# Performance work log

Measured on AMD Instinct MI355X. Metric: run time of the kernel, lower is better.

## Reference

```python
import jax, jax.numpy as jnp
import numpy as np

B, K, H, E = 16384, 5, 512, 512


def setup_inputs() -> dict:
    key = jax.random.key(0)
    ks = jax.random.split(key, 6)
    return {
        "query": jax.random.normal(ks[0], (B, H), dtype=jnp.float32),
        "topics": jax.random.normal(ks[1], (B, K, E), dtype=jnp.float32),
        "coverage_vector": jax.random.uniform(ks[2], (B, K), dtype=jnp.float32),
        "Ua": jax.random.normal(ks[3], (H, E), dtype=jnp.float32) * (1.0 / np.sqrt(E)),
        "Wa": jax.random.normal(ks[4], (H, H), dtype=jnp.float32) * (1.0 / np.sqrt(H)),
        "va_w": jax.random.normal(ks[5], (1, H), dtype=jnp.float32) * (1.0 / np.sqrt(H)),
        "va_b": jnp.zeros((1,), dtype=jnp.float32),
    }


def reference(query, topics, coverage_vector, Ua, Wa, va_w, va_b):
    # proj_key for all topics at once: [B, K, H]
    proj_keys = jnp.einsum("bke,he->bkh", topics, Ua)
    # Faithful to original: query is re-projected by Wa each loop iteration,
    # so step i uses Wa^(i+1) @ query.
    q = query
    scores = []
    for i in range(topics.shape[1]):  # K is small & fixed (topics)
        q = q @ Wa.T  # [B, H]
        s = jnp.tanh(q + proj_keys[:, i, :]) @ va_w.T + va_b  # [B, 1]
        scores.append(s[:, 0] * coverage_vector[:, i])  # [B]
    scores = jnp.stack(scores, axis=1)  # [B, K]
    alphas = jax.nn.softmax(scores, axis=1)  # [B, K]
    mt = jnp.einsum("bk,bke->be", alphas, topics)  # [B, E]
    return (mt, alphas)
```

## Files before the change

kernel.cpp:

```cpp
#include <hip/hip_runtime.h>
#include <hip/hip_bf16.h>
#include <stdint.h>

#define B_SZ 16384
#define K_SZ 5
#define H_SZ 512
#define E_SZ 512

typedef _Float16 f16;
typedef _Float16 f16x8 __attribute__((ext_vector_type(8)));
typedef float    f32x4 __attribute__((ext_vector_type(4)));

__device__ __forceinline__ void gload_lds16(const void* g, void* l) {
  __builtin_amdgcn_global_load_lds(
      (const __attribute__((address_space(1))) unsigned int*)g,
      (__attribute__((address_space(3))) unsigned int*)l, 16, 0, 0);
}

__device__ __forceinline__ float fast_tanh(float x) {
  float e = __expf(-2.f * fabsf(x));
  float r = (1.f - e) / (1.f + e);
  return copysignf(r, x);
}

__global__ __launch_bounds__(256)
void prep_all(const float* __restrict__ Wa, const float* __restrict__ Ua,
              const float* __restrict__ query, f16* __restrict__ Wbig0,
              f16* __restrict__ Ua_h, f16* __restrict__ WaT,
              f16* __restrict__ q0h, unsigned* __restrict__ bar) {
  const int t = threadIdx.x;
  const int bb = blockIdx.x;
  if (bb == 0 && t == 0) *bar = 0u;
  if (bb < 128) {
    size_t o = ((size_t)bb * 256 + t) * 8;
    float4 a = *(const float4*)(Wa + o);
    float4 b = *(const float4*)(Wa + o + 4);
    union { f16 h[8]; uint4 u; } u;
    u.h[0] = (f16)a.x; u.h[1] = (f16)a.y; u.h[2] = (f16)a.z; u.h[3] = (f16)a.w;
    u.h[4] = (f16)b.x; u.h[5] = (f16)b.y; u.h[6] = (f16)b.z; u.h[7] = (f16)b.w;
    *(uint4*)(Wbig0 + o) = u.u;
  } else if (bb < 256) {
    size_t o = ((size_t)(bb - 128) * 256 + t) * 8;
    float4 a = *(const float4*)(Ua + o);
    float4 b = *(const float4*)(Ua + o + 4);
    union { f16 h[8]; uint4 u; } u;
    u.h[0] = (f16)a.x; u.h[1] = (f16)a.y; u.h[2] = (f16)a.z; u.h[3] = (f16)a.w;
    u.h[4] = (f16)b.x; u.h[5] = (f16)b.y; u.h[6] = (f16)b.z; u.h[7] = (f16)b.w;
    *(uint4*)(Ua_h + o) = u.u;
  } else if (bb < 512) {
    __shared__ float tile[32][33];
    int blk = bb - 256;
    int bx = blk & 15, by = blk >> 4;
    int tx = t & 31, ty = t >> 5;
    #pragma unroll
    for (int i = 0; i < 32; i += 8)
      tile[ty + i][tx] = Wa[(size_t)(by * 32 + ty + i) * 512 + bx * 32 + tx];
    __syncthreads();
    #pragma unroll
    for (int i = 0; i < 32; i += 8)
      WaT[(size_t)(bx * 32 + ty + i) * 512 + by * 32 + tx] =
          (f16)tile[tx][ty + i];
  } else {
    size_t o = ((size_t)(bb - 512) * 256 + t) * 8;
    float4 a = *(const float4*)(query + o);
    float4 b = *(const float4*)(query + o + 4);
    union { f16 h[8]; uint4 u; } u;
    u.h[0] = (f16)a.x; u.h[1] = (f16)a.y; u.h[2] = (f16)a.z; u.h[3] = (f16)a.w;
    u.h[4] = (f16)b.x; u.h[5] = (f16)b.y; u.h[6] = (f16)b.z; u.h[7] = (f16)b.w;
    *(uint4*)(q0h + o) = u.u;
  }
}

__device__ __forceinline__ void gbar(unsigned* cnt, unsigned target) {
  __syncthreads();
  if (threadIdx.x == 0) {
    __threadfence();
    __hip_atomic_fetch_add(cnt, 1u, __ATOMIC_ACQ_REL, __HIP_MEMORY_SCOPE_AGENT);
    while (__hip_atomic_load(cnt, __ATOMIC_ACQUIRE,
                             __HIP_MEMORY_SCOPE_AGENT) < target)
      __builtin_amdgcn_s_sleep(2);
    __threadfence();
  }
  __syncthreads();
}

__global__ __launch_bounds__(256)
void power_chain(const f16* __restrict__ WaT, f16* __restrict__ Wbig,
                 unsigned* __restrict__ bar) {
  __shared__ f16 As[128 * 32];
  __shared__ f16 Bs[128 * 32];
  const int t = threadIdx.x, l = t & 63, wid = t >> 6;
  const int wm = wid >> 1, wn = wid & 1;
  const int mt = blockIdx.x >> 2, nt = blockIdx.x & 3;
  const int m0 = mt * 128, n0 = nt * 128;
  const int lrow = l & 15, lk = (l >> 4) * 8;

  for (int j = 1; j < K_SZ; ++j) {
    const f16* A = Wbig + (size_t)(j - 1) * (512 * 512);
    f16* Y = Wbig + (size_t)j * (512 * 512);
    f32x4 acc[4][4] = {};
    for (int k0 = 0; k0 < 512; k0 += 32) {
      #pragma unroll
      for (int p = 0; p < 2; ++p) {
        int c = p * 256 + t, row = c >> 2, seg = c & 3;
        gload_lds16(WaT + (size_t)(n0 + row) * 512 + k0 + seg * 8,
                    (char*)Bs + c * 16);
        gload_lds16(A + (size_t)(m0 + row) * 512 + k0 + seg * 8,
                    (char*)As + c * 16);
      }
      __syncthreads();
      f16x8 af[4], bf[4];
      #pragma unroll
      for (int mi = 0; mi < 4; ++mi)
        af[mi] = *(const f16x8*)(As + (wm * 64 + mi * 16 + lrow) * 32 + lk);
      #pragma unroll
      for (int ni = 0; ni < 4; ++ni)
        bf[ni] = *(const f16x8*)(Bs + (wn * 64 + ni * 16 + lrow) * 32 + lk);
      #pragma unroll
      for (int mi = 0; mi < 4; ++mi)
        #pragma unroll
        for (int ni = 0; ni < 4; ++ni)
          acc[mi][ni] = __builtin_amdgcn_mfma_f32_16x16x32_f16(
              af[mi], bf[ni], acc[mi][ni], 0, 0, 0);
      __syncthreads();
    }
    #pragma unroll
    for (int mi = 0; mi < 4; ++mi)
      #pragma unroll
      for (int j2 = 0; j2 < 4; ++j2) {
        size_t row = m0 + wm * 64 + mi * 16 + ((l >> 4) << 2) + j2;
        #pragma unroll
        for (int ni = 0; ni < 4; ++ni)
          Y[row * 512 + n0 + wn * 64 + ni * 16 + lrow] = (f16)acc[mi][ni][j2];
      }
    if (j < K_SZ - 1) gbar(bar, 16u * (unsigned)j);
  }
}

__global__ __launch_bounds__(256)
void fused_score_gemm(const float* __restrict__ topics,
                      const f16* __restrict__ q0h,
                      const f16* __restrict__ Ua_h,
                      const f16* __restrict__ Wbig,
                      const float* __restrict__ va_w,
                      float* __restrict__ partials) {
  __shared__ f16 As[2][128 * 32];
  __shared__ f16 Bs[2][128 * 32];
  const int t = threadIdx.x;
  const int l = t & 63, wid = t >> 6;
  const int wm = wid >> 1, wn = wid & 1;
  int bid = blockIdx.x;
  const int nwg = gridDim.x;
  bid = (bid & 7) * (nwg >> 3) + (bid >> 3);
  const int kq = bid >> 9;
  const int rem = bid & 511;
  const int mt = rem >> 2, nt = rem & 3;
  const size_t m0 = (size_t)mt * 128;
  const int n0 = nt * 128;
  const int lrow = l & 15;
  const int lk = (l >> 4) * 8;
  const f16* Pk = Wbig + (size_t)kq * (512 * 512);

  const float* tA = topics + ((m0 + (t >> 3)) * K_SZ + kq) * (size_t)E_SZ +
                    (t & 7) * 4;
  const int ldsA1 = (t >> 3) * 64 + (t & 7) * 8;
  const f16* tB1 = Ua_h + (size_t)(n0 + (t >> 2)) * 512 + (t & 3) * 8;
  const f16* tB2 = Pk + (size_t)(n0 + (t >> 2)) * 512 + (t & 3) * 8;
  const f16* tA2 = q0h + (m0 + (t >> 2)) * (size_t)H_SZ + (t & 3) * 8;

  float4 areg[4];
  f32x4 acc[4][4] = {};

  auto stage1 = [&](int k0, int buf) {
    #pragma unroll
    for (int p = 0; p < 2; ++p)
      gload_lds16(tB1 + (size_t)p * 64 * 512 + k0,
                  (char*)Bs[buf] + (p * 256 + t) * 16);
    #pragma unroll
    for (int p = 0; p < 4; ++p)
      areg[p] = *(const float4*)(tA + (size_t)p * 32 * K_SZ * E_SZ + k0);
  };
  auto write1 = [&](int buf) {
    #pragma unroll
    for (int p = 0; p < 4; ++p) {
      union { f16 h[4]; uint2 u; } cv;
      cv.h[0] = (f16)areg[p].x; cv.h[1] = (f16)areg[p].y;
      cv.h[2] = (f16)areg[p].z; cv.h[3] = (f16)areg[p].w;
      *(uint2*)((char*)As[buf] + p * 2048 + ldsA1) = cv.u;
    }
  };
  auto stage2 = [&](int k0, int buf) {
    #pragma unroll
    for (int p = 0; p < 2; ++p) {
      gload_lds16(tB2 + (size_t)p * 64 * 512 + k0,
                  (char*)Bs[buf] + (p * 256 + t) * 16);
      gload_lds16(tA2 + (size_t)p * 64 * H_SZ + k0,
                  (char*)As[buf] + (p * 256 + t) * 16);
    }
  };
  auto compute = [&](int buf) {
    f16x8 af[4], bf[4];
    #pragma unroll
    for (int mi = 0; mi < 4; ++mi)
      af[mi] = *(const f16x8*)(As[buf] + (wm * 64 + mi * 16 + lrow) * 32 + lk);
    #pragma unroll
    for (int ni = 0; ni < 4; ++ni)
      bf[ni] = *(const f16x8*)(Bs[buf] + (wn * 64 + ni * 16 + lrow) * 32 + lk);
    #pragma unroll
    for (int mi = 0; mi < 4; ++mi)
      #pragma unroll
      for (int ni = 0; ni < 4; ++ni)
        acc[mi][ni] = __builtin_amdgcn_mfma_f32_16x16x32_f16(
            af[mi], bf[ni], acc[mi][ni], 0, 0, 0);
  };

  stage1(0, 0);
  write1(0);
  __syncthreads();

  #pragma unroll 2
  for (int i = 0; i < 16; ++i) {
    const int cur = i & 1;
    if (i < 15) stage1((i + 1) * 32, cur ^ 1);
    else        stage2(0, cur ^ 1);
    compute(cur);
    if (i < 15) write1(cur ^ 1);
    __syncthreads();
  }
  #pragma unroll 2
  for (int i = 0; i < 16; ++i) {
    const int cur = i & 1;
    if (i < 15) stage2((i + 1) * 32, cur ^ 1);
    compute(cur);
    __syncthreads();
  }

  const int colbase = n0 + wn * 64 + lrow;
  float va4[4];
  #pragma unroll
  for (int ni = 0; ni < 4; ++ni) va4[ni] = va_w[colbase + ni * 16];

  #pragma unroll
  for (int mi = 0; mi < 4; ++mi) {
    #pragma unroll
    for (int j = 0; j < 4; ++j) {
      float s = 0.f;
      #pragma unroll
      for (int ni = 0; ni < 4; ++ni)
        s += va4[ni] * fast_tanh(acc[mi][ni][j]);
      #pragma unroll
      for (int m = 1; m < 16; m <<= 1) s += __shfl_xor(s, m);
      if (lrow == 0) {
        int row = (int)m0 + wm * 64 + mi * 16 + ((l >> 4) << 2) + j;
        partials[(size_t)(nt * 2 + wn) * (K_SZ * B_SZ) + kq * B_SZ + row] = s;
      }
    }
  }
}

__global__ __launch_bounds__(256)
void finalize2(const float* __restrict__ partials,
               const float* __restrict__ topics, const float* __restrict__ cov,
               const float* __restrict__ va_b, float* __restrict__ out) {
  const int wid = threadIdx.x >> 6, l = threadIdx.x & 63;
  const size_t b = (size_t)blockIdx.x * 4 + wid;
  const float vb = va_b[0];

  float s[K_SZ];
  #pragma unroll
  for (int k = 0; k < K_SZ; ++k) {
    float raw = 0.f;
    #pragma unroll
    for (int sl = 0; sl < 8; ++sl)
      raw += partials[(size_t)sl * (K_SZ * B_SZ) + k * B_SZ + b];
    s[k] = (raw + vb) * cov[b * K_SZ + k];
  }

  float m = s[0];
  #pragma unroll
  for (int k = 1; k < K_SZ; ++k) m = fmaxf(m, s[k]);
  float a[K_SZ], d = 0.f;
  #pragma unroll
  for (int k = 0; k < K_SZ; ++k) { a[k] = __expf(s[k] - m); d += a[k]; }
  float inv = 1.f / d;
  #pragma unroll
  for (int k = 0; k < K_SZ; ++k) a[k] *= inv;

  float acc0[4] = {}, acc1[4] = {};
  #pragma unroll
  for (int k = 0; k < K_SZ; ++k) {
    const float* tp = topics + (b * K_SZ + k) * E_SZ + l * 8;
    float4 t0 = *(const float4*)tp;
    float4 t1 = *(const float4*)(tp + 4);
    acc0[0] += a[k] * t0.x; acc0[1] += a[k] * t0.y;
    acc0[2] += a[k] * t0.z; acc0[3] += a[k] * t0.w;
    acc1[0] += a[k] * t1.x; acc1[1] += a[k] * t1.y;
    acc1[2] += a[k] * t1.z; acc1[3] += a[k] * t1.w;
  }
  float* mo = out + b * E_SZ + l * 8;
  *(float4*)mo       = make_float4(acc0[0], acc0[1], acc0[2], acc0[3]);
  *(float4*)(mo + 4) = make_float4(acc1[0], acc1[1], acc1[2], acc1[3]);
  if (l < K_SZ) {
    float av = (l == 0) ? a[0] : (l == 1) ? a[1] : (l == 2) ? a[2]
               : (l == 3) ? a[3] : a[4];
    out[(size_t)B_SZ * E_SZ + b * K_SZ + l] = av;
  }
}

extern "C" void kernel_launch(void* const* d_in, const int* in_sizes, int n_in,
                              void* d_out, int out_size, void* d_ws, size_t ws_size,
                              hipStream_t stream) {
  const float* query  = (const float*)d_in[0];
  const float* topics = (const float*)d_in[1];
  const float* cov    = (const float*)d_in[2];
  const float* Ua     = (const float*)d_in[3];
  const float* Wa     = (const float*)d_in[4];
  const float* va_w   = (const float*)d_in[5];
  const float* va_b   = (const float*)d_in[6];
  float* out = (float*)d_out;

  char* ws = (char*)d_ws;
  size_t off = 0;
  auto alloc = [&](size_t bytes) -> char* {
    char* p = ws + off;
    off += (bytes + 255) & ~(size_t)255;
    return p;
  };
  f16* q0h   = (f16*)alloc((size_t)B_SZ * H_SZ * 2);
  f16* Ua_h  = (f16*)alloc((size_t)H_SZ * E_SZ * 2);
  f16* WaT   = (f16*)alloc((size_t)H_SZ * H_SZ * 2);
  f16* Wbig  = (f16*)alloc((size_t)K_SZ * H_SZ * H_SZ * 2);
  float* partials = (float*)alloc((size_t)8 * K_SZ * B_SZ * 4);
  unsigned* bar   = (unsigned*)alloc(256);

  prep_all<<<4608, 256, 0, stream>>>(Wa, Ua, query, Wbig, Ua_h, WaT, q0h, bar);
  power_chain<<<16, 256, 0, stream>>>(WaT, Wbig, bar);
  fused_score_gemm<<<K_SZ * (B_SZ / 128) * (H_SZ / 128), 256, 0, stream>>>(
      topics, q0h, Ua_h, Wbig, va_w, partials);
  finalize2<<<B_SZ / 4, 256, 0, stream>>>(partials, topics, cov, va_b, out);
}
```

Baseline: 481.0 us.

## Split-K Wa power chain across 256 blocks and pre-convert topics to fp16

The serial 16-block power chain that computed Wa^2..Wa^5 is replaced by a 256-block split-K scheme with fp32 partial buffers, reductions and global barriers. It also uses repeated squaring (Wa^2 transposed, then Wa^3 and Wa^4, then Wa^5), which cuts the chain to three dependent GEMM levels. Topics are converted to fp16 once in the prep kernel, so the score GEMM can use direct global-to-LDS loads and finalize reads half the bytes. The score GEMM loses its double buffering in exchange, and the extra fp16 topics pass adds traffic. Rounding topics to fp16 also lowers the precision of the mt output.

```diff
diff --git a/kernel.cpp b/kernel.cpp
--- a/kernel.cpp
+++ b/kernel.cpp
@@ -6,6 +6,7 @@
 #define K_SZ 5
 #define H_SZ 512
 #define E_SZ 512
+#define MSZ (512 * 512)
 
 typedef _Float16 f16;
 typedef _Float16 f16x8 __attribute__((ext_vector_type(8)));
@@ -23,30 +24,30 @@
   return copysignf(r, x);
 }
 
+__device__ __forceinline__ void cvt8(const float* src, f16* dst) {
+  float4 a = *(const float4*)src;
+  float4 b = *(const float4*)(src + 4);
+  union { f16 h[8]; uint4 u; } u;
+  u.h[0] = (f16)a.x; u.h[1] = (f16)a.y; u.h[2] = (f16)a.z; u.h[3] = (f16)a.w;
+  u.h[4] = (f16)b.x; u.h[5] = (f16)b.y; u.h[6] = (f16)b.z; u.h[7] = (f16)b.w;
+  *(uint4*)dst = u.u;
+}
+
 __global__ __launch_bounds__(256)
 void prep_all(const float* __restrict__ Wa, const float* __restrict__ Ua,
-              const float* __restrict__ query, f16* __restrict__ Wbig0,
-              f16* __restrict__ Ua_h, f16* __restrict__ WaT,
-              f16* __restrict__ q0h, unsigned* __restrict__ bar) {
+              const float* __restrict__ query, const float* __restrict__ topics,
+              f16* __restrict__ Wbig0, f16* __restrict__ Ua_h,
+              f16* __restrict__ WaT, f16* __restrict__ q0h,
+              f16* __restrict__ topics_h, unsigned* __restrict__ bar) {
   const int t = threadIdx.x;
   const int bb = blockIdx.x;
   if (bb == 0 && t == 0) *bar = 0u;
   if (bb < 128) {
     size_t o = ((size_t)bb * 256 + t) * 8;
-    float4 a = *(const float4*)(Wa + o);
-    float4 b = *(const float4*)(Wa + o + 4);
-    union { f16 h[8]; uint4 u; } u;
-    u.h[0] = (f16)a.x; u.h[1] = (f16)a.y; u.h[2] = (f16)a.z; u.h[3] = (f16)a.w;
-    u.h[4] = (f16)b.x; u.h[5] = (f16)b.y; u.h[6] = (f16)b.z; u.h[7] = (f16)b.w;
-    *(uint4*)(Wbig0 + o) = u.u;
+    cvt8(Wa + o, Wbig0 + o);
   } else if (bb < 256) {
     size_t o = ((size_t)(bb - 128) * 256 + t) * 8;
-    float4 a = *(const float4*)(Ua + o);
-    float4 b = *(const float4*)(Ua + o + 4);
-    union { f16 h[8]; uint4 u; } u;
-    u.h[0] = (f16)a.x; u.h[1] = (f16)a.y; u.h[2] = (f16)a.z; u.h[3] = (f16)a.w;
-    u.h[4] = (f16)b.x; u.h[5] = (f16)b.y; u.h[6] = (f16)b.z; u.h[7] = (f16)b.w;
-    *(uint4*)(Ua_h + o) = u.u;
+    cvt8(Ua + o, Ua_h + o);
   } else if (bb < 512) {
     __shared__ float tile[32][33];
     int blk = bb - 256;
@@ -60,14 +61,12 @@
     for (int i = 0; i < 32; i += 8)
       WaT[(size_t)(bx * 32 + ty + i) * 512 + by * 32 + tx] =
           (f16)tile[tx][ty + i];
+  } else if (bb < 4608) {
+    size_t o = ((size_t)(bb - 512) * 256 + t) * 8;
+    cvt8(query + o, q0h + o);
   } else {
-    size_t o = ((size_t)(bb - 512) * 256 + t) * 8;
-    float4 a = *(const float4*)(query + o);
-    float4 b = *(const float4*)(query + o + 4);
-    union { f16 h[8]; uint4 u; } u;
-    u.h[0] = (f16)a.x; u.h[1] = (f16)a.y; u.h[2] = (f16)a.z; u.h[3] = (f16)a.w;
-    u.h[4] = (f16)b.x; u.h[5] = (f16)b.y; u.h[6] = (f16)b.z; u.h[7] = (f16)b.w;
-    *(uint4*)(q0h + o) = u.u;
+    size_t o = ((size_t)(bb - 4608) * 256 + t) * 8;
+    cvt8(topics + o, topics_h + o);
   }
 }
 
@@ -85,25 +84,28 @@
 }
 
 __global__ __launch_bounds__(256)
-void power_chain(const f16* __restrict__ WaT, f16* __restrict__ Wbig,
+void power_split(f16* __restrict__ Wbig, const f16* __restrict__ WaT,
+                 f16* __restrict__ W2T, float* __restrict__ part,
                  unsigned* __restrict__ bar) {
   __shared__ f16 As[128 * 32];
   __shared__ f16 Bs[128 * 32];
   const int t = threadIdx.x, l = t & 63, wid = t >> 6;
   const int wm = wid >> 1, wn = wid & 1;
-  const int mt = blockIdx.x >> 2, nt = blockIdx.x & 3;
-  const int m0 = mt * 128, n0 = nt * 128;
   const int lrow = l & 15, lk = (l >> 4) * 8;
-
-  for (int j = 1; j < K_SZ; ++j) {
-    const f16* A = Wbig + (size_t)(j - 1) * (512 * 512);
-    f16* Y = Wbig + (size_t)j * (512 * 512);
+  const int bid = blockIdx.x;
+  float* p0 = part;
+  float* p1 = part + (size_t)8 * MSZ;
+
+  auto spk = [&](const f16* A, const f16* W, float* P, int blk) {
+    const int tile = blk >> 3, ks = blk & 7;
+    const int m0 = (tile >> 2) * 128, n0 = (tile & 3) * 128;
     f32x4 acc[4][4] = {};
-    for (int k0 = 0; k0 < 512; k0 += 32) {
+    for (int ki = 0; ki < 2; ++ki) {
+      const int k0 = ks * 64 + ki * 32;
       #pragma unroll
       for (int p = 0; p < 2; ++p) {
         int c = p * 256 + t, row = c >> 2, seg = c & 3;
-        gload_lds16(WaT + (size_t)(n0 + row) * 512 + k0 + seg * 8,
+        gload_lds16(W + (size_t)(n0 + row) * 512 + k0 + seg * 8,
                     (char*)Bs + c * 16);
         gload_lds16(A + (size_t)(m0 + row) * 512 + k0 + seg * 8,
                     (char*)As + c * 16);
@@ -124,28 +126,68 @@
               af[mi], bf[ni], acc[mi][ni], 0, 0, 0);
       __syncthreads();
     }
+    float* Ps = P + (size_t)ks * MSZ;
     #pragma unroll
     for (int mi = 0; mi < 4; ++mi)
       #pragma unroll
-      for (int j2 = 0; j2 < 4; ++j2) {
-        size_t row = m0 + wm * 64 + mi * 16 + ((l >> 4) << 2) + j2;
+      for (int j = 0; j < 4; ++j) {
+        int row = m0 + wm * 64 + mi * 16 + ((l >> 4) << 2) + j;
         #pragma unroll
         for (int ni = 0; ni < 4; ++ni)
-          Y[row * 512 + n0 + wn * 64 + ni * 16 + lrow] = (f16)acc[mi][ni][j2];
+          Ps[(size_t)row * 512 + n0 + wn * 64 + ni * 16 + lrow] =
+              acc[mi][ni][j];
       }
-    if (j < K_SZ - 1) gbar(bar, 16u * (unsigned)j);
-  }
+  };
+  auto reduceg = [&](const float* P, f16* D, int blk) {
+    const int base = (blk * 256 + t) * 8;
+    float s[8] = {};
+    #pragma unroll
+    for (int sl = 0; sl < 8; ++sl) {
+      const float* q = P + (size_t)sl * MSZ + base;
+      float4 a = *(const float4*)q;
+      float4 b = *(const float4*)(q + 4);
+      s[0] += a.x; s[1] += a.y; s[2] += a.z; s[3] += a.w;
+      s[4] += b.x; s[5] += b.y; s[6] += b.z; s[7] += b.w;
+    }
+    union { f16 h[8]; uint4 u; } cv;
+    #pragma unroll
+    for (int j = 0; j < 8; ++j) cv.h[j] = (f16)s[j];
+    *(uint4*)(D + base) = cv.u;
+  };
+
+  f16* Wa1 = Wbig;
+  f16* Wa2 = Wbig + MSZ;
+  f16* Wa3 = Wbig + 2 * (size_t)MSZ;
+  f16* Wa4 = Wbig + 3 * (size_t)MSZ;
+  f16* Wa5 = Wbig + 4 * (size_t)MSZ;
+  unsigned tg = 0;
+
+  if (bid < 128) spk(Wa1, WaT, p0, bid);
+  else           spk(WaT, Wa1, p1, bid - 128);
+  gbar(bar, tg += 256);
+  if (bid < 128) reduceg(p0, Wa2, bid);
+  else           reduceg(p1, W2T, bid - 128);
+  gbar(bar, tg += 256);
+  if (bid < 128) spk(Wa2, WaT, p0, bid);
+  else           spk(Wa2, W2T, p1, bid - 128);
+  gbar(bar, tg += 256);
+  if (bid < 128) reduceg(p0, Wa3, bid);
+  else           reduceg(p1, Wa4, bid - 128);
+  gbar(bar, tg += 256);
+  if (bid < 128) spk(Wa4, WaT, p0, bid);
+  gbar(bar, tg += 256);
+  if (bid < 128) reduceg(p0, Wa5, bid);
 }
 
 __global__ __launch_bounds__(256)
-void fused_score_gemm(const float* __restrict__ topics,
+void fused_score_gemm(const f16* __restrict__ topics_h,
                       const f16* __restrict__ q0h,
                       const f16* __restrict__ Ua_h,
                       const f16* __restrict__ Wbig,
                       const float* __restrict__ va_w,
                       float* __restrict__ partials) {
-  __shared__ f16 As[2][128 * 32];
-  __shared__ f16 Bs[2][128 * 32];
+  __shared__ f16 As[128 * 32];
+  __shared__ f16 Bs[128 * 32];
   const int t = threadIdx.x;
   const int l = t & 63, wid = t >> 6;
   const int wm = wid >> 1, wn = wid & 1;
@@ -159,53 +201,24 @@
   const int n0 = nt * 128;
   const int lrow = l & 15;
   const int lk = (l >> 4) * 8;
-  const f16* Pk = Wbig + (size_t)kq * (512 * 512);
-
-  const float* tA = topics + ((m0 + (t >> 3)) * K_SZ + kq) * (size_t)E_SZ +
-                    (t & 7) * 4;
-  const int ldsA1 = (t >> 3) * 64 + (t & 7) * 8;
-  const f16* tB1 = Ua_h + (size_t)(n0 + (t >> 2)) * 512 + (t & 3) * 8;
-  const f16* tB2 = Pk + (size_t)(n0 + (t >> 2)) * 512 + (t & 3) * 8;
-  const f16* tA2 = q0h + (m0 + (t >> 2)) * (size_t)H_SZ + (t & 3) * 8;
-
-  float4 areg[4];
+  const f16* Pk = Wbig + (size_t)kq * MSZ;
+
+  const int srow = t >> 2, sseg = (t & 3) * 8;
+  const f16* tA1 = topics_h + ((m0 + srow) * K_SZ + kq) * (size_t)E_SZ + sseg;
+  const f16* tB1 = Ua_h + (size_t)(n0 + srow) * 512 + sseg;
+  const f16* tA2 = q0h + (m0 + srow) * (size_t)H_SZ + sseg;
+  const f16* tB2 = Pk + (size_t)(n0 + srow) * 512 + sseg;
+
   f32x4 acc[4][4] = {};
 
-  auto stage1 = [&](int k0, int buf) {
-    #pragma unroll
-    for (int p = 0; p < 2; ++p)
-      gload_lds16(tB1 + (size_t)p * 64 * 512 + k0,
-                  (char*)Bs[buf] + (p * 256 + t) * 16);
-    #pragma unroll
-    for (int p = 0; p < 4; ++p)
-      areg[p] = *(const float4*)(tA + (size_t)p * 32 * K_SZ * E_SZ + k0);
-  };
-  auto write1 = [&](int buf) {
-    #pragma unroll
-    for (int p = 0; p < 4; ++p) {
-      union { f16 h[4]; uint2 u; } cv;
-      cv.h[0] = (f16)areg[p].x; cv.h[1] = (f16)areg[p].y;
-      cv.h[2] = (f16)areg[p].z; cv.h[3] = (f16)areg[p].w;
-      *(uint2*)((char*)As[buf] + p * 2048 + ldsA1) = cv.u;
-    }
-  };
-  auto stage2 = [&](int k0, int buf) {
-    #pragma unroll
-    for (int p = 0; p < 2; ++p) {
-      gload_lds16(tB2 + (size_t)p * 64 * 512 + k0,
-                  (char*)Bs[buf] + (p * 256 + t) * 16);
-      gload_lds16(tA2 + (size_t)p * 64 * H_SZ + k0,
-                  (char*)As[buf] + (p * 256 + t) * 16);
-    }
-  };
-  auto compute = [&](int buf) {
+  auto compute = [&]() {
     f16x8 af[4], bf[4];
     #pragma unroll
     for (int mi = 0; mi < 4; ++mi)
-      af[mi] = *(const f16x8*)(As[buf] + (wm * 64 + mi * 16 + lrow) * 32 + lk);
+      af[mi] = *(const f16x8*)(As + (wm * 64 + mi * 16 + lrow) * 32 + lk);
     #pragma unroll
     for (int ni = 0; ni < 4; ++ni)
-      bf[ni] = *(const f16x8*)(Bs[buf] + (wn * 64 + ni * 16 + lrow) * 32 + lk);
+      bf[ni] = *(const f16x8*)(Bs + (wn * 64 + ni * 16 + lrow) * 32 + lk);
     #pragma unroll
     for (int mi = 0; mi < 4; ++mi)
       #pragma unroll
@@ -214,24 +227,28 @@
             af[mi], bf[ni], acc[mi][ni], 0, 0, 0);
   };
 
-  stage1(0, 0);
-  write1(0);
-  __syncthreads();
-
-  #pragma unroll 2
-  for (int i = 0; i < 16; ++i) {
-    const int cur = i & 1;
-    if (i < 15) stage1((i + 1) * 32, cur ^ 1);
-    else        stage2(0, cur ^ 1);
-    compute(cur);
-    if (i < 15) write1(cur ^ 1);
-    __syncthreads();
-  }
-  #pragma unroll 2
-  for (int i = 0; i < 16; ++i) {
-    const int cur = i & 1;
-    if (i < 15) stage2((i + 1) * 32, cur ^ 1);
-    compute(cur);
+  for (int k0 = 0; k0 < 512; k0 += 32) {
+    #pragma unroll
+    for (int p = 0; p < 2; ++p) {
+      gload_lds16(tB1 + (size_t)p * 64 * 512 + k0,
+                  (char*)Bs + (p * 256 + t) * 16);
+      gload_lds16(tA1 + (size_t)p * 64 * (K_SZ * E_SZ) + k0,
+                  (char*)As + (p * 256 + t) * 16);
+    }
+    __syncthreads();
+    compute();
+    __syncthreads();
+  }
+  for (int k0 = 0; k0 < 512; k0 += 32) {
+    #pragma unroll
+    for (int p = 0; p < 2; ++p) {
+      gload_lds16(tB2 + (size_t)p * 64 * 512 + k0,
+                  (char*)Bs + (p * 256 + t) * 16);
+      gload_lds16(tA2 + (size_t)p * 64 * H_SZ + k0,
+                  (char*)As + (p * 256 + t) * 16);
+    }
+    __syncthreads();
+    compute();
     __syncthreads();
   }
 
@@ -260,7 +277,7 @@
 
 __global__ __launch_bounds__(256)
 void finalize2(const float* __restrict__ partials,
-               const float* __restrict__ topics, const float* __restrict__ cov,
+               const f16* __restrict__ topics_h, const float* __restrict__ cov,
                const float* __restrict__ va_b, float* __restrict__ out) {
   const int wid = threadIdx.x >> 6, l = threadIdx.x & 63;
   const size_t b = (size_t)blockIdx.x * 4 + wid;
@@ -286,20 +303,16 @@
   #pragma unroll
   for (int k = 0; k < K_SZ; ++k) a[k] *= inv;
 
-  float acc0[4] = {}, acc1[4] = {};
+  float accv[8] = {};
   #pragma unroll
   for (int k = 0; k < K_SZ; ++k) {
-    const float* tp = topics + (b * K_SZ + k) * E_SZ + l * 8;
-    float4 t0 = *(const float4*)tp;
-    float4 t1 = *(const float4*)(tp + 4);
-    acc0[0] += a[k] * t0.x; acc0[1] += a[k] * t0.y;
-    acc0[2] += a[k] * t0.z; acc0[3] += a[k] * t0.w;
-    acc1[0] += a[k] * t1.x; acc1[1] += a[k] * t1.y;
-    acc1[2] += a[k] * t1.z; acc1[3] += a[k] * t1.w;
+    f16x8 tv = *(const f16x8*)(topics_h + (b * K_SZ + k) * E_SZ + l * 8);
+    #pragma unroll
+    for (int j = 0; j < 8; ++j) accv[j] += a[k] * (float)tv[j];
   }
   float* mo = out + b * E_SZ + l * 8;
-  *(float4*)mo       = make_float4(acc0[0], acc0[1], acc0[2], acc0[3]);
-  *(float4*)(mo + 4) = make_float4(acc1[0], acc1[1], acc1[2], acc1[3]);
+  *(float4*)mo       = make_float4(accv[0], accv[1], accv[2], accv[3]);
+  *(float4*)(mo + 4) = make_float4(accv[4], accv[5], accv[6], accv[7]);
   if (l < K_SZ) {
     float av = (l == 0) ? a[0] : (l == 1) ? a[1] : (l == 2) ? a[2]
                : (l == 3) ? a[3] : a[4];
@@ -326,16 +339,20 @@
     off += (bytes + 255) & ~(size_t)255;
     return p;
   };
-  f16* q0h   = (f16*)alloc((size_t)B_SZ * H_SZ * 2);
-  f16* Ua_h  = (f16*)alloc((size_t)H_SZ * E_SZ * 2);
-  f16* WaT   = (f16*)alloc((size_t)H_SZ * H_SZ * 2);
-  f16* Wbig  = (f16*)alloc((size_t)K_SZ * H_SZ * H_SZ * 2);
+  f16* topics_h = (f16*)alloc((size_t)B_SZ * K_SZ * E_SZ * 2);
+  f16* q0h      = (f16*)alloc((size_t)B_SZ * H_SZ * 2);
+  f16* Ua_h     = (f16*)alloc((size_t)MSZ * 2);
+  f16* WaT      = (f16*)alloc((size_t)MSZ * 2);
+  f16* Wbig     = (f16*)alloc((size_t)K_SZ * MSZ * 2);
+  f16* W2T      = (f16*)alloc((size_t)MSZ * 2);
+  float* part   = (float*)alloc((size_t)16 * MSZ * 4);
   float* partials = (float*)alloc((size_t)8 * K_SZ * B_SZ * 4);
-  unsigned* bar   = (unsigned*)alloc(256);
-
-  prep_all<<<4608, 256, 0, stream>>>(Wa, Ua, query, Wbig, Ua_h, WaT, q0h, bar);
-  power_chain<<<16, 256, 0, stream>>>(WaT, Wbig, bar);
+  unsigned* bar = (unsigned*)alloc(256);
+
+  prep_all<<<25088, 256, 0, stream>>>(Wa, Ua, query, topics, Wbig, Ua_h, WaT,
+                                      q0h, topics_h, bar);
+  power_split<<<256, 256, 0, stream>>>(Wbig, WaT, W2T, part, bar);
   fused_score_gemm<<<K_SZ * (B_SZ / 128) * (H_SZ / 128), 256, 0, stream>>>(
-      topics, q0h, Ua_h, Wbig, va_w, partials);
-  finalize2<<<B_SZ / 4, 256, 0, stream>>>(partials, topics, cov, va_b, out);
-}
+      topics_h, q0h, Ua_h, Wbig, va_w, partials);
+  finalize2<<<B_SZ / 4, 256, 0, stream>>>(partials, topics_h, cov, va_b, out);
+}
```

New measurement: 611.1 us. 1.27x slower.
